# Performance work log

Measured on AMD Instinct MI355X. Metric: run time of the kernel, lower is better.

## Reference

```python
import jax, jax.numpy as jnp
import numpy as np
from jax import lax

K = 5
SCALE = 100.0
IN_CHN = 128
OUT_CHN = 128
KS = 3
STRIDE = 1
PAD = 1
N_W = OUT_CHN * IN_CHN * KS * KS


def setup_inputs() -> dict:
    key = jax.random.key(0)
    k1, k2, k3, k4, k5 = jax.random.split(key, 5)
    x = jax.random.normal(k1, (32, IN_CHN, 56, 56), dtype=jnp.float32)
    Alpha = jax.random.uniform(k2, (OUT_CHN, 1, 1), dtype=jnp.float32)
    # xavier-normal-ish init for M, Z
    M = jax.random.normal(k3, (OUT_CHN, IN_CHN, KS, KS), dtype=jnp.float32) * 0.05
    Z = jax.random.normal(k4, (K, OUT_CHN, IN_CHN, KS, KS), dtype=jnp.float32) * 0.05
    # rv ~ N(0, 1/sqrt(scale)) of shape (1, K); sample is all-zeros so the random branch is taken
    rv = jax.random.normal(k5, (1, K), dtype=jnp.float32) / np.float32(np.sqrt(SCALE))
    return {"x": x, "Alpha": Alpha, "M": M, "Z": Z, "rv": rv}


def reference(x, Alpha, M, Z, rv):
    # --- SDP weight synthesis (normalization is done under no_grad in torch) ---
    m = M.reshape(N_W)                # (N,)
    z = Z.reshape(K, N_W)             # (K, N)
    A = m * m + jnp.sum(z * z, axis=0) / SCALE
    inv = lax.rsqrt(A)
    m_n = m * inv
    z_n = z * inv
    w = (rv @ z_n + m_n).reshape(OUT_CHN, IN_CHN, KS, KS)  # (O,I,k,k)
    # --- sign binarization of weights and activations (ReCU) ---
    bw = jnp.sign(w)
    ba = jnp.sign(x)
    # --- conv2d, NCHW/OIHW ---
    out = lax.conv_general_dilated(
        ba, bw,
        window_strides=(STRIDE, STRIDE),
        padding=[(PAD, PAD), (PAD, PAD)],
        dimension_numbers=("NCHW", "OIHW", "NCHW"),
    )
    out = out * Alpha  # Alpha (O,1,1) broadcasts over (B,O,H,W)
    return out
```

## Files before the change

### kernel.cpp

```cpp
#include <hip/hip_runtime.h>
#include <stdint.h>

typedef unsigned int u32;
typedef unsigned long long u64;
typedef float f32x4 __attribute__((ext_vector_type(4)));

#define HW      3136
#define PADW    58
#define PADHW   3364

#define WB_OFF   0
#define BF_OFF   18432
#define N2A_OFF  23040
#define AB_OFF   23552

#define NB_W     128
#define NB_A     392
#define NB_R     29

__global__ __launch_bounds__(256) void k_prep(
    const float* __restrict__ x, const float* __restrict__ Alpha,
    const float* __restrict__ M, const float* __restrict__ Z,
    const float* __restrict__ rv, char* __restrict__ ws)
{
  int t = threadIdx.x;
  if (blockIdx.x < NB_W) {
    u32*   wb  = (u32*)(ws + WB_OFF);
    float* Bf  = (float*)(ws + BF_OFF);
    float* n2a = (float*)(ws + N2A_OFF);
    __shared__ float sw[1152];
    __shared__ u32 sbits[36];
    __shared__ int spc[9];
    int o = blockIdx.x;
    float r0 = rv[0], r1 = rv[1], r2 = rv[2], r3 = rv[3], r4 = rv[4];
    const float4* M4 = (const float4*)M;
    const float4* Z4 = (const float4*)Z;
    float4* sw4 = (float4*)sw;

    for (int j = t; j < 288; j += 256) {
      float4 a = M4[o * 288 + j];
      float4 z;
      z = Z4[0 * 36864 + o * 288 + j];
      a.x = fmaf(r0, z.x, a.x); a.y = fmaf(r0, z.y, a.y);
      a.z = fmaf(r0, z.z, a.z); a.w = fmaf(r0, z.w, a.w);
      z = Z4[1 * 36864 + o * 288 + j];
      a.x = fmaf(r1, z.x, a.x); a.y = fmaf(r1, z.y, a.y);
      a.z = fmaf(r1, z.z, a.z); a.w = fmaf(r1, z.w, a.w);
      z = Z4[2 * 36864 + o * 288 + j];
      a.x = fmaf(r2, z.x, a.x); a.y = fmaf(r2, z.y, a.y);
      a.z = fmaf(r2, z.z, a.z); a.w = fmaf(r2, z.w, a.w);
      z = Z4[3 * 36864 + o * 288 + j];
      a.x = fmaf(r3, z.x, a.x); a.y = fmaf(r3, z.y, a.y);
      a.z = fmaf(r3, z.z, a.z); a.w = fmaf(r3, z.w, a.w);
      z = Z4[4 * 36864 + o * 288 + j];
      a.x = fmaf(r4, z.x, a.x); a.y = fmaf(r4, z.y, a.y);
      a.z = fmaf(r4, z.z, a.z); a.w = fmaf(r4, z.w, a.w);
      sw4[j] = a;
    }
    __syncthreads();

    if (t < 36) {
      int tap = t >> 2;
      int wd  = t & 3;
      u32 bits = 0;
#pragma unroll
      for (int c = 0; c < 32; ++c) {
        float v = sw[(wd * 32 + c) * 9 + tap];
        bits |= (v > 0.0f ? 1u : 0u) << c;
      }
      wb[(o * 9 + tap) * 4 + wd] = bits;
      sbits[t] = bits;
    }
    __syncthreads();
    if (t < 9)
      spc[t] = __popc(sbits[4 * t]) + __popc(sbits[4 * t + 1])
             + __popc(sbits[4 * t + 2]) + __popc(sbits[4 * t + 3]);
    __syncthreads();
    if (t < 9) {
      int ht = t / 3, wt = t - ht * 3;
      int corr = 0;
#pragma unroll
      for (int tap = 0; tap < 9; ++tap) {
        int dh = tap / 3, dw = tap - dh * 3;
        int inv = ((ht == 0) & (dh == 0)) | ((ht == 2) & (dh == 2)) |
                  ((wt == 0) & (dw == 0)) | ((wt == 2) & (dw == 2));
        if (inv) corr += 128 - 2 * spc[tap];
      }
      Bf[t * 128 + o] = (float)(1152 - corr) * Alpha[o];
    }
    if (t == 0) n2a[o] = -2.0f * Alpha[o];
  } else if (blockIdx.x < NB_W + NB_A) {
    u32* abw = (u32*)(ws + AB_OFF);
    int idx = (blockIdx.x - NB_W) * 256 + t;
    int bg  = idx / 784;
    int q   = idx - bg * 784;
    int b   = bg >> 2;
    int g   = bg & 3;
    int h   = q / 14;
    int w0  = (q - h * 14) * 4;

    const float4* X4 = (const float4*)x
        + ((size_t)b * 128 + g * 32) * (HW / 4) + q;
    u32 m0 = 0, m1 = 0, m2 = 0, m3 = 0;
#pragma unroll
    for (int c = 0; c < 32; ++c) {
      float4 f = X4[(size_t)c * (HW / 4)];
      m0 |= (f.x > 0.0f ? 1u : 0u) << c;
      m1 |= (f.y > 0.0f ? 1u : 0u) << c;
      m2 |= (f.z > 0.0f ? 1u : 0u) << c;
      m3 |= (f.w > 0.0f ? 1u : 0u) << c;
    }
    size_t base = ((size_t)b * PADHW + (h + 1) * PADW + (w0 + 1)) * 4 + g;
    abw[base]      = m0;
    abw[base + 4]  = m1;
    abw[base + 8]  = m2;
    abw[base + 12] = m3;
  } else {
    uint4* ab4 = (uint4*)(ws + AB_OFF);
    int e = (blockIdx.x - NB_W - NB_A) * 256 + t;
    if (e >= 32 * 228) return;
    int b  = e / 228;
    int r  = e - b * 228;
    int pp;
    if      (r < 58)  pp = r;
    else if (r < 116) pp = 57 * PADW + (r - 58);
    else {
      int s = r - 116;
      pp = (1 + (s >> 1)) * PADW + ((s & 1) ? 57 : 0);
    }
    ab4[(size_t)b * PADHW + pp] = make_uint4(0, 0, 0, 0);
  }
}

__global__ __launch_bounds__(64) void k_conv(
    const char* __restrict__ ws, float* __restrict__ out)
{
  const uint4*  ab  = (const uint4*)(ws + AB_OFF);
  const uint4*  wbg = (const uint4*)(ws + WB_OFF);
  const float*  BfG = (const float*)(ws + BF_OFF);
  const float*  n2a = (const float*)(ws + N2A_OFF);

  __shared__ uint4 swb[144];
  __shared__ float sBf[9][16];
  __shared__ float sn2a[16];
  int tid = threadIdx.x;
  int o0  = blockIdx.y * 16;
#pragma unroll
  for (int j = tid; j < 144; j += 64) {
    swb[j] = wbg[o0 * 9 + j];
    (&sBf[0][0])[j] = BfG[(j >> 4) * 128 + o0 + (j & 15)];
  }
  if (tid < 16) sn2a[tid] = n2a[o0 + tid];
  __syncthreads();

  int q  = blockIdx.x * 64 + tid;
  int b  = q / 784;
  int r  = q - b * 784;
  int h  = r / 14;
  int w4 = r - h * 14;
  int w0 = w4 * 4;

  const uint4* ap = ab + (size_t)b * PADHW + (size_t)h * PADW + w0;
  u32 A[3][6][4];
#pragma unroll
  for (int rr = 0; rr < 3; ++rr)
#pragma unroll
    for (int cc = 0; cc < 6; ++cc) {
      uint4 v = ap[(size_t)rr * PADW + cc];
      A[rr][cc][0] = v.x; A[rr][cc][1] = v.y;
      A[rr][cc][2] = v.z; A[rr][cc][3] = v.w;
    }

  int ht  = (h == 0) ? 0 : (h == 55 ? 6 : 3);
  int cl0 = ht + ((w0 == 0) ? 0 : 1);
  int cl1 = ht + 1;
  int cl3 = ht + ((w0 == 52) ? 2 : 1);

  float* outp = out + ((size_t)b * 128 + o0) * HW + h * 56 + w0;

#pragma unroll 4
  for (int oi = 0; oi < 16; ++oi) {
    int s0 = 0, s1 = 0, s2 = 0, s3 = 0;
#pragma unroll
    for (int dh = 0; dh < 3; ++dh)
#pragma unroll
      for (int dw = 0; dw < 3; ++dw) {
        uint4 wv = swb[oi * 9 + dh * 3 + dw];
#pragma unroll
        for (int k = 0; k < 4; ++k) {
          u32 wk = (&wv.x)[k];
          s0 += __popc(A[dh][dw + 0][k] ^ wk);
          s1 += __popc(A[dh][dw + 1][k] ^ wk);
          s2 += __popc(A[dh][dw + 2][k] ^ wk);
          s3 += __popc(A[dh][dw + 3][k] ^ wk);
        }
      }
    float na = sn2a[oi];
    f32x4 ov;
    ov.x = fmaf((float)s0, na, sBf[cl0][oi]);
    ov.y = fmaf((float)s1, na, sBf[cl1][oi]);
    ov.z = fmaf((float)s2, na, sBf[cl1][oi]);
    ov.w = fmaf((float)s3, na, sBf[cl3][oi]);
    __builtin_nontemporal_store(ov, (f32x4*)(outp + (size_t)oi * HW));
  }
}

extern "C" void kernel_launch(void* const* d_in, const int* in_sizes, int n_in,
                              void* d_out, int out_size, void* d_ws, size_t ws_size,
                              hipStream_t stream)
{
  const float* x     = (const float*)d_in[0];
  const float* Alpha = (const float*)d_in[1];
  const float* M     = (const float*)d_in[2];
  const float* Z     = (const float*)d_in[3];
  const float* rv    = (const float*)d_in[4];
  float* out         = (float*)d_out;
  char*  ws          = (char*)d_ws;

  k_prep<<<NB_W + NB_A + NB_R, 256, 0, stream>>>(x, Alpha, M, Z, rv, ws);
  k_conv<<<dim3(392, 8), 64, 0, stream>>>(ws, out);
}
```

Measured before the change: 140.4 us.

## Map one output pixel per thread in binary conv, widen blocks to 256

The conv kernel moves from four horizontally adjacent output pixels per thread to one pixel per thread, with 256-thread blocks over the same grid. Each thread now loads a 3x3 neighborhood of packed activation words instead of 3x6, giving fewer registers and more threads to hide latency. The cost is lost horizontal reuse of activation loads (about 2x more loads per output), more LDS weight reads per popcount, and scalar stores in place of 16-byte vector stores.

```diff
diff --git a/kernel.cpp b/kernel.cpp
--- a/kernel.cpp
+++ b/kernel.cpp
@@ -3,7 +3,6 @@
 
 typedef unsigned int u32;
 typedef unsigned long long u64;
-typedef float f32x4 __attribute__((ext_vector_type(4)));
 
 #define HW      3136
 #define PADW    58
@@ -132,7 +131,7 @@
   }
 }
 
-__global__ __launch_bounds__(64) void k_conv(
+__global__ __launch_bounds__(256) void k_conv(
     const char* __restrict__ ws, float* __restrict__ out)
 {
   const uint4*  ab  = (const uint4*)(ws + AB_OFF);
@@ -143,65 +142,52 @@
   __shared__ uint4 swb[144];
   __shared__ float sBf[9][16];
   __shared__ float sn2a[16];
-  int tid = threadIdx.x;
-  int o0  = blockIdx.y * 16;
-#pragma unroll
-  for (int j = tid; j < 144; j += 64) {
-    swb[j] = wbg[o0 * 9 + j];
-    (&sBf[0][0])[j] = BfG[(j >> 4) * 128 + o0 + (j & 15)];
+  int t  = threadIdx.x;
+  int o0 = blockIdx.y * 16;
+  if (t < 144) {
+    swb[t] = wbg[o0 * 9 + t];
+    (&sBf[0][0])[t] = BfG[(t >> 4) * 128 + o0 + (t & 15)];
   }
-  if (tid < 16) sn2a[tid] = n2a[o0 + tid];
+  if (t < 16) sn2a[t] = n2a[o0 + t];
   __syncthreads();
 
-  int q  = blockIdx.x * 64 + tid;
-  int b  = q / 784;
-  int r  = q - b * 784;
-  int h  = r / 14;
-  int w4 = r - h * 14;
-  int w0 = w4 * 4;
-
-  const uint4* ap = ab + (size_t)b * PADHW + (size_t)h * PADW + w0;
-  u32 A[3][6][4];
+  int gp = blockIdx.x * 256 + t;
+  int b  = gp / HW;
+  int p  = gp - b * HW;
+  int h  = p / 56;
+  int w  = p - h * 56;
+
+  const uint4* ap = ab + (size_t)b * PADHW + (size_t)h * PADW + w;
+  u32 A[3][3][4];
 #pragma unroll
   for (int rr = 0; rr < 3; ++rr)
 #pragma unroll
-    for (int cc = 0; cc < 6; ++cc) {
+    for (int cc = 0; cc < 3; ++cc) {
       uint4 v = ap[(size_t)rr * PADW + cc];
       A[rr][cc][0] = v.x; A[rr][cc][1] = v.y;
       A[rr][cc][2] = v.z; A[rr][cc][3] = v.w;
     }
 
-  int ht  = (h == 0) ? 0 : (h == 55 ? 6 : 3);
-  int cl0 = ht + ((w0 == 0) ? 0 : 1);
-  int cl1 = ht + 1;
-  int cl3 = ht + ((w0 == 52) ? 2 : 1);
-
-  float* outp = out + ((size_t)b * 128 + o0) * HW + h * 56 + w0;
+  int cl = ((h == 0) ? 0 : (h == 55 ? 6 : 3))
+         + ((w == 0) ? 0 : (w == 55 ? 2 : 1));
+
+  float* outp = out + ((size_t)b * 128 + o0) * HW + p;
 
 #pragma unroll 4
   for (int oi = 0; oi < 16; ++oi) {
-    int s0 = 0, s1 = 0, s2 = 0, s3 = 0;
+    int s = 0;
 #pragma unroll
     for (int dh = 0; dh < 3; ++dh)
 #pragma unroll
       for (int dw = 0; dw < 3; ++dw) {
         uint4 wv = swb[oi * 9 + dh * 3 + dw];
-#pragma unroll
-        for (int k = 0; k < 4; ++k) {
-          u32 wk = (&wv.x)[k];
-          s0 += __popc(A[dh][dw + 0][k] ^ wk);
-          s1 += __popc(A[dh][dw + 1][k] ^ wk);
-          s2 += __popc(A[dh][dw + 2][k] ^ wk);
-          s3 += __popc(A[dh][dw + 3][k] ^ wk);
-        }
+        s += __popc(A[dh][dw][0] ^ wv.x);
+        s += __popc(A[dh][dw][1] ^ wv.y);
+        s += __popc(A[dh][dw][2] ^ wv.z);
+        s += __popc(A[dh][dw][3] ^ wv.w);
       }
-    float na = sn2a[oi];
-    f32x4 ov;
-    ov.x = fmaf((float)s0, na, sBf[cl0][oi]);
-    ov.y = fmaf((float)s1, na, sBf[cl1][oi]);
-    ov.z = fmaf((float)s2, na, sBf[cl1][oi]);
-    ov.w = fmaf((float)s3, na, sBf[cl3][oi]);
-    __builtin_nontemporal_store(ov, (f32x4*)(outp + (size_t)oi * HW));
+    float ov = fmaf((float)s, sn2a[oi], sBf[cl][oi]);
+    __builtin_nontemporal_store(ov, outp + (size_t)oi * HW);
   }
 }
 
@@ -218,5 +204,5 @@
   char*  ws          = (char*)d_ws;
 
   k_prep<<<NB_W + NB_A + NB_R, 256, 0, stream>>>(x, Alpha, M, Z, rv, ws);
-  k_conv<<<dim3(392, 8), 64, 0, stream>>>(ws, out);
+  k_conv<<<dim3(392, 8), 256, 0, stream>>>(ws, out);
 }
```

Result: faster. 137.4 us (-2.1%).
